# Performance work log

Measured on AMD Instinct MI355X. Metric: run time of the kernel, lower is better.

## Reference

```python
import jax, jax.numpy as jnp
import numpy as np

NUM_RELATIONS = 8
NUM_BASES = 4
IN_CH, HID, OUT_CH = 128, 64, 64
N_NODES, N_EDGES = 50000, 500000


def rgcn_conv(x, edge_src, edge_dst, edge_type, basis, comp, root, bias):
    """PyG RGCNConv with basis decomposition and per-relation mean aggregation.
    basis: [B, in, out], comp: [R, B], root: [in, out], bias: [out].
    W_r = sum_b comp[r, b] * basis[b]; msg_e = x[src_e] @ W_{type_e};
    aggregate mean over incoming edges per (node, relation), sum over relations,
    then add root transform and bias.
    """
    n = x.shape[0]
    out_dim = basis.shape[2]
    # Project once through all bases: [N, B, out]  (cheap: B=4)
    h = jnp.einsum('ni,bio->nbo', x, basis)
    # Per-edge message: contract gathered basis features with per-edge comp coeffs
    msg = jnp.einsum('eb,ebo->eo', comp[edge_type], h[edge_src])  # [E, out]
    # Mean aggregation per (dst, relation): segment id = dst*R + relation
    seg = edge_dst * NUM_RELATIONS + edge_type
    sums = jax.ops.segment_sum(msg, seg, num_segments=n * NUM_RELATIONS)
    cnt = jax.ops.segment_sum(jnp.ones((msg.shape[0], 1), msg.dtype), seg,
                              num_segments=n * NUM_RELATIONS)
    mean = sums / jnp.maximum(cnt, 1.0)
    agg = mean.reshape(n, NUM_RELATIONS, out_dim).sum(axis=1)
    return agg + x @ root + bias


def setup_inputs() -> dict:
    key = jax.random.key(0)
    ks = jax.random.split(key, 12)
    s1 = 1.0 / np.sqrt(IN_CH)
    s2 = 1.0 / np.sqrt(HID)
    return {
        'x': jax.random.normal(ks[0], (N_NODES, IN_CH), jnp.float32),
        'edge_index': jax.random.randint(ks[1], (2, N_EDGES), 0, N_NODES, jnp.int64),
        'edge_type': jax.random.randint(ks[2], (N_EDGES,), 0, NUM_RELATIONS, jnp.int64),
        'basis1': jax.random.normal(ks[3], (NUM_BASES, IN_CH, HID), jnp.float32) * s1,
        'comp1': jax.random.normal(ks[4], (NUM_RELATIONS, NUM_BASES), jnp.float32) * 0.5,
        'root1': jax.random.normal(ks[5], (IN_CH, HID), jnp.float32) * s1,
        'bias1': jnp.zeros((HID,), jnp.float32),
        'basis2': jax.random.normal(ks[6], (NUM_BASES, HID, OUT_CH), jnp.float32) * s2,
        'comp2': jax.random.normal(ks[7], (NUM_RELATIONS, NUM_BASES), jnp.float32) * 0.5,
        'root2': jax.random.normal(ks[8], (HID, OUT_CH), jnp.float32) * s2,
        'bias2': jnp.zeros((OUT_CH,), jnp.float32),
    }


def reference(x, edge_index, edge_type, basis1, comp1, root1, bias1,
              basis2, comp2, root2, bias2):
    src, dst = edge_index[0], edge_index[1]
    h = rgcn_conv(x, src, dst, edge_type, basis1, comp1, root1, bias1)
    h = jax.nn.relu(h)
    out = rgcn_conv(h, src, dst, edge_type, basis2, comp2, root2, bias2)
    return out
```

## Files before the change

kernel.cpp:

```cpp
#include <hip/hip_runtime.h>
#include <cstddef>

#define NREL 8
#define SCAN_TILE 4096

typedef __bf16 bf16x8 __attribute__((ext_vector_type(8)));
typedef float f32x4 __attribute__((ext_vector_type(4)));

__device__ __forceinline__ unsigned f2bf_u(float f) {
    unsigned u = __float_as_uint(f);
    u += 0x7FFFu + ((u >> 16) & 1u);
    return u >> 16;
}
__device__ __forceinline__ short f2bf(float f) { return (short)f2bf_u(f); }
__device__ __forceinline__ int pack2bf(float lo, float hi) {
    return (int)(f2bf_u(lo) | (f2bf_u(hi) << 16));
}
__device__ __forceinline__ float bfval(unsigned short g) {
    return __uint_as_float((unsigned)g << 16);
}

template<int K>
__device__ __forceinline__ void wfrag_body(const float* __restrict__ basis,
                                           const float* __restrict__ root,
                                           const float* __restrict__ comp,
                                           short* __restrict__ Wf, int tid)
{
    constexpr int NK = K / 32;
    int lane = tid & 63, slot = tid >> 6;
    int ks = slot % NK, t = slot / NK;
    int kg = lane >> 4, lr = lane & 15;
    int k0 = ks * 32 + kg * 8;
    union { short s[8]; int4 v; } u;
#pragma unroll
    for (int e = 0; e < 8; ++e) {
        int k = k0 + e;
        float v;
        if (t < 32) {
            int rr = t >> 2, ch = (t & 3) * 16 + lr;
            v = comp[rr * 4 + 0] * basis[((size_t)0 * K + k) * 64 + ch]
              + comp[rr * 4 + 1] * basis[((size_t)1 * K + k) * 64 + ch]
              + comp[rr * 4 + 2] * basis[((size_t)2 * K + k) * 64 + ch]
              + comp[rr * 4 + 3] * basis[((size_t)3 * K + k) * 64 + ch];
        } else {
            v = root[(size_t)k * 64 + (t - 32) * 16 + lr];
        }
        u.s[e] = f2bf(v);
    }
    *(int4*)(Wf + (size_t)tid * 8) = u.v;
}

__device__ __forceinline__ void afrag_body128(const float* __restrict__ x,
                                              short* __restrict__ xf, int N, int tid)
{
    int lane = tid & 63, slot = tid >> 6;
    int ks = slot & 3, rt = slot >> 2;
    int kg = lane >> 4, lr = lane & 15;
    int row = rt * 16 + lr, k = ks * 32 + kg * 8;
    union { short s[8]; int4 v; } u;
    if (row < N) {
        const float* xp = x + (size_t)row * 128 + k;
        float4 a = *(const float4*)xp;
        float4 b = *(const float4*)(xp + 4);
        u.s[0] = f2bf(a.x); u.s[1] = f2bf(a.y); u.s[2] = f2bf(a.z); u.s[3] = f2bf(a.w);
        u.s[4] = f2bf(b.x); u.s[5] = f2bf(b.y); u.s[6] = f2bf(b.z); u.s[7] = f2bf(b.w);
    } else {
        u.v = make_int4(0, 0, 0, 0);
    }
    *(int4*)(xf + (size_t)tid * 8) = u.v;
}

__global__ __launch_bounds__(256) void prep_kernel(
    const float* __restrict__ basis1, const float* __restrict__ root1,
    const float* __restrict__ comp1,  const float* __restrict__ basis2,
    const float* __restrict__ root2,  const float* __restrict__ comp2,
    const float* __restrict__ x,
    short* __restrict__ Wf1, short* __restrict__ Wf2, short* __restrict__ xf1,
    int4* __restrict__ zp, int zn16, int* __restrict__ offsN,
    int E, int N, int NT)
{
    int b = blockIdx.x;
    const int zb = (zn16 + 255) >> 8;
    if (b < zb) {
        int i = b * 256 + threadIdx.x;
        if (i < zn16) zp[i] = make_int4(0, 0, 0, 0);
        if (b == 0 && threadIdx.x == 0) *offsN = E;
        return;
    }
    b -= zb;
    if (b < 36) { wfrag_body<128>(basis1, root1, comp1, Wf1, b * 256 + threadIdx.x); return; }
    b -= 36;
    if (b < 18) { wfrag_body<64>(basis2, root2, comp2, Wf2, b * 256 + threadIdx.x); return; }
    b -= 18;
    int tid = b * 256 + threadIdx.x;
    if (tid < NT * 256) afrag_body128(x, xf1, N, tid);
}

__global__ __launch_bounds__(256) void hist_kernel(const int* __restrict__ dst,
                                                   const int* __restrict__ et,
                                                   int* __restrict__ cnt8, int E)
{
    int e = blockIdx.x * 256 + threadIdx.x;
    if (e < E) atomicAdd(&cnt8[dst[e] * NREL + et[e]], 1);
}

__global__ __launch_bounds__(256) void scan_part(const int* __restrict__ cnt8,
                                                 int* __restrict__ tsum, int n)
{
    int base = blockIdx.x * SCAN_TILE;
    int s = 0;
    for (int i = threadIdx.x; i < SCAN_TILE; i += 256) {
        int idx = base + i;
        if (idx < n) {
            int4 a = ((const int4*)cnt8)[idx * 2];
            int4 b = ((const int4*)cnt8)[idx * 2 + 1];
            s += a.x + a.y + a.z + a.w + b.x + b.y + b.z + b.w;
        }
    }
    for (int d = 1; d < 64; d <<= 1) s += __shfl_xor(s, d, 64);
    __shared__ int ws[4];
    if ((threadIdx.x & 63) == 0) ws[threadIdx.x >> 6] = s;
    __syncthreads();
    if (threadIdx.x == 0) tsum[blockIdx.x] = ws[0] + ws[1] + ws[2] + ws[3];
}

__global__ __launch_bounds__(256) void scan_final(const int* __restrict__ cnt8,
                                                  const int* __restrict__ tsum,
                                                  int* __restrict__ offs, int n)
{
    const int lane = threadIdx.x & 63, wid = threadIdx.x >> 6;
    int tbase = 0;
    for (int i = 0; i < blockIdx.x; ++i) tbase += tsum[i];
    int base = blockIdx.x * SCAN_TILE + threadIdx.x * 16;
    int v[16]; int s = 0;
#pragma unroll
    for (int j = 0; j < 16; ++j) {
        int idx = base + j;
        int dv = 0;
        if (idx < n) {
            int4 a = ((const int4*)cnt8)[idx * 2];
            int4 b = ((const int4*)cnt8)[idx * 2 + 1];
            dv = a.x + a.y + a.z + a.w + b.x + b.y + b.z + b.w;
        }
        v[j] = dv; s += dv;
    }
    int inc = s;
    for (int d = 1; d < 64; d <<= 1) {
        int t = __shfl_up(inc, d, 64);
        if (lane >= d) inc += t;
    }
    __shared__ int wsum[4];
    if (lane == 63) wsum[wid] = inc;
    __syncthreads();
    int run = tbase + (inc - s);
    for (int k = 0; k < wid; ++k) run += wsum[k];
#pragma unroll
    for (int j = 0; j < 16; ++j) {
        int idx = base + j;
        if (idx < n) offs[idx] = run;
        run += v[j];
    }
}

__global__ __launch_bounds__(256) void scatter_kernel(const int* __restrict__ src,
                                                      const int* __restrict__ dst,
                                                      const int* __restrict__ et,
                                                      const int* __restrict__ offs,
                                                      int* __restrict__ cursor,
                                                      const int* __restrict__ cnt8,
                                                      int2* __restrict__ edgeP, int E)
{
    int e = blockIdx.x * 256 + threadIdx.x;
    if (e >= E) return;
    int d = dst[e], r = et[e], s = src[e];
    int c = cnt8[d * NREL + r];
    float inv = 1.0f / (float)(c > 1 ? c : 1);
    int pos = offs[d] + atomicAdd(&cursor[d], 1);
    edgeP[pos] = make_int2(s * NREL + r, __float_as_int(inv));
}

template<int K>
__global__ __launch_bounds__(256) void gemm_mfma(const short* __restrict__ xf,
                                                 const short* __restrict__ Wf,
                                                 const float* __restrict__ bias,
                                                 short* __restrict__ hr,
                                                 float* __restrict__ yinit,
                                                 int N, int gblk)
{
    constexpr int NK = K / 32;
    __shared__ short lds[12 * NK * 512];

    const int w = threadIdx.x >> 6, lane = threadIdx.x & 63;
    const int kg = lane >> 4, lr = lane & 15;
    const int g0 = blockIdx.y * 3;

    {
        const int4* gsrc = (const int4*)(Wf + (size_t)g0 * 4 * NK * 512);
        int4* ldst = (int4*)lds;
        for (int i = threadIdx.x; i < 12 * NK * 64; i += 256)
            ldst[i] = gsrc[i];
    }

    float b0 = bias[lr], b1 = bias[16 + lr], b2 = bias[32 + lr], b3 = bias[48 + lr];

    __syncthreads();

    for (int bx = blockIdx.x; bx < gblk; bx += gridDim.x) {
        const int rt = bx * 4 + w;

        bf16x8 afrag[NK];
        const short* ap = xf + ((size_t)rt * NK * 64 + lane) * 8;
#pragma unroll
        for (int ks = 0; ks < NK; ++ks)
            afrag[ks] = *(const bf16x8*)(ap + ks * 512);

        f32x4 acc[12];
#pragma unroll
        for (int t = 0; t < 12; ++t) acc[t] = (f32x4){0.f, 0.f, 0.f, 0.f};

#pragma unroll
        for (int tt = 0; tt < 12; ++tt) {
#pragma unroll
            for (int ks = 0; ks < NK; ++ks) {
                bf16x8 bfrag = *(const bf16x8*)(lds + (tt * NK + ks) * 512 + lane * 8);
                acc[tt] = __builtin_amdgcn_mfma_f32_16x16x32_bf16(afrag[ks], bfrag,
                                                                  acc[tt], 0, 0, 0);
            }
        }

        const int drow0 = rt * 16 + kg * 4;
#pragma unroll
        for (int r = 0; r < 4; ++r) {
            int dr = drow0 + r;
            if (dr >= N) break;
#pragma unroll
            for (int gg = 0; gg < 3; ++gg) {
                int g = g0 + gg;
                if (g < 8) {
                    int u0 = pack2bf(acc[gg * 4 + 0][r], acc[gg * 4 + 1][r]);
                    int u1 = pack2bf(acc[gg * 4 + 2][r], acc[gg * 4 + 3][r]);
                    *(int2*)(hr + (size_t)dr * 512 + g * 64 + lr * 4) = make_int2(u0, u1);
                } else {
                    float4 o = make_float4(acc[gg * 4 + 0][r] + b0, acc[gg * 4 + 1][r] + b1,
                                           acc[gg * 4 + 2][r] + b2, acc[gg * 4 + 3][r] + b3);
                    *(float4*)(yinit + (size_t)dr * 64 + lr * 4) = o;
                }
            }
        }
    }
}

template<bool BF16OUT>
__global__ __launch_bounds__(256) void agg_kernel(const int* __restrict__ offs,
                                                  const int2* __restrict__ edgeP,
                                                  const short* __restrict__ hr,
                                                  const float* __restrict__ init,
                                                  float* __restrict__ outF,
                                                  short* __restrict__ outB, int N)
{
    const int dst = blockIdx.x * 4 + (threadIdx.x >> 6);
    const int l = threadIdx.x & 63;
    if (dst >= N) return;

    const unsigned short* hp = (const unsigned short*)hr;
    float acc = init[(size_t)dst * 64 + l];
    int e0 = offs[dst], e1 = offs[dst + 1];

    int e = e0;
    for (; e + 3 < e1; e += 4) {
        int2 p0 = edgeP[e],     p1 = edgeP[e + 1];
        int2 p2 = edgeP[e + 2], p3 = edgeP[e + 3];
        unsigned short g0 = hp[(size_t)p0.x * 64 + l];
        unsigned short g1 = hp[(size_t)p1.x * 64 + l];
        unsigned short g2 = hp[(size_t)p2.x * 64 + l];
        unsigned short g3 = hp[(size_t)p3.x * 64 + l];
        acc = fmaf(bfval(g0), __int_as_float(p0.y), acc);
        acc = fmaf(bfval(g1), __int_as_float(p1.y), acc);
        acc = fmaf(bfval(g2), __int_as_float(p2.y), acc);
        acc = fmaf(bfval(g3), __int_as_float(p3.y), acc);
    }
    for (; e < e1; ++e) {
        int2 p0 = edgeP[e];
        unsigned short g0 = hp[(size_t)p0.x * 64 + l];
        acc = fmaf(bfval(g0), __int_as_float(p0.y), acc);
    }

    int tc = (l & 3) * 16 + (l >> 2);
    if (BF16OUT) {
        int rt2 = dst >> 4, lr2 = dst & 15;
        int ks2 = tc >> 5, kg2 = (tc >> 3) & 3, e2 = tc & 7;
        outB[(((size_t)rt2 * 2 + ks2) * 64 + kg2 * 16 + lr2) * 8 + e2] =
            f2bf(fmaxf(acc, 0.f));
    } else {
        outF[(size_t)dst * 64 + tc] = acc;
    }
}

extern "C" void kernel_launch(void* const* d_in, const int* in_sizes, int n_in,
                              void* d_out, int out_size, void* d_ws, size_t ws_size,
                              hipStream_t stream)
{
    const float* x      = (const float*)d_in[0];
    const int*   ei     = (const int*)d_in[1];
    const int*   et     = (const int*)d_in[2];
    const float* basis1 = (const float*)d_in[3];
    const float* comp1  = (const float*)d_in[4];
    const float* root1  = (const float*)d_in[5];
    const float* bias1  = (const float*)d_in[6];
    const float* basis2 = (const float*)d_in[7];
    const float* comp2  = (const float*)d_in[8];
    const float* root2  = (const float*)d_in[9];
    const float* bias2  = (const float*)d_in[10];
    float* out = (float*)d_out;

    const int N = in_sizes[0] / 128;
    const int E = in_sizes[2];
    const int* src  = ei;
    const int* dstp = ei + E;

    const int gblk = (N + 63) / 64;
    const int NT   = gblk * 4;
    const int ablk = (N + 3) / 4;

    char* p = (char*)d_ws;
    auto carve = [&](size_t bytes) -> char* {
        char* q = p; p += (bytes + 255) & ~(size_t)255; return q;
    };
    int*   cursor  = (int*)carve((size_t)N * 4);
    int*   cnt8    = (int*)carve((size_t)N * NREL * 4);
    char*  zend    = p;
    int*   offs    = (int*)carve((size_t)(N + 1) * 4);
    int*   tsum    = (int*)carve(256 * 4);
    int2*  edgeP   = (int2*)carve((size_t)E * 8);
    short* Wf1     = (short*)carve((size_t)36 * 4 * 64 * 8 * 2);
    short* Wf2     = (short*)carve((size_t)36 * 2 * 64 * 8 * 2);
    float* yinit   = (float*)carve((size_t)N * 64 * 4);
    short* xf1     = (short*)carve((size_t)NT * 4 * 64 * 8 * 2);
    short* xf2     = (short*)carve((size_t)NT * 2 * 64 * 8 * 2);
    short* hr      = (short*)carve((size_t)N * 512 * 2);

    const int zn16 = (int)((zend - (char*)cursor) / 16);
    const int zb   = (zn16 + 255) / 256;
    const int ntiles = (N + SCAN_TILE - 1) / SCAN_TILE;

    prep_kernel<<<zb + 36 + 18 + NT, 256, 0, stream>>>(
        basis1, root1, comp1, basis2, root2, comp2, x,
        Wf1, Wf2, xf1, (int4*)cursor, zn16, offs + N, E, N, NT);

    hist_kernel<<<(E + 255) / 256, 256, 0, stream>>>(dstp, et, cnt8, E);
    scan_part<<<ntiles, 256, 0, stream>>>(cnt8, tsum, N);
    scan_final<<<ntiles, 256, 0, stream>>>(cnt8, tsum, offs, N);
    scatter_kernel<<<(E + 255) / 256, 256, 0, stream>>>(src, dstp, et, offs, cursor,
                                                        cnt8, edgeP, E);

    gemm_mfma<128><<<dim3(196, 3), 256, 0, stream>>>(xf1, Wf1, bias1, hr, yinit, N, gblk);
    agg_kernel<true><<<ablk, 256, 0, stream>>>(offs, edgeP, hr, yinit, nullptr, xf2, N);

    gemm_mfma<64><<<dim3(196, 3), 256, 0, stream>>>(xf2, Wf2, bias2, hr, yinit, N, gblk);
    agg_kernel<false><<<ablk, 256, 0, stream>>>(offs, edgeP, hr, yinit, out, nullptr, N);
}
```

Baseline: 189.8 us.

## Fuse histogram into prep, scatter with GEMM1, split edges across waves

Moves zeroing into its own kernel so the edge histogram can run inside the prep kernel. The edge scatter is fused with the first GEMM, which is made non-persistent and reads weight fragments straight from global memory instead of staging them in LDS. The root-plus-bias term is stored as bf16 instead of fp32, which cuts bandwidth at some precision cost. Aggregation now uses two waves per destination node that split the edge list and combine through LDS, aiming for more parallel gathers on nodes with many edges.

```diff
diff --git a/kernel.cpp b/kernel.cpp
--- a/kernel.cpp
+++ b/kernel.cpp
@@ -18,6 +18,14 @@
 }
 __device__ __forceinline__ float bfval(unsigned short g) {
     return __uint_as_float((unsigned)g << 16);
+}
+
+__global__ __launch_bounds__(256) void zero_kernel(int4* __restrict__ p, int n16,
+                                                   int* __restrict__ offsN, int E)
+{
+    int i = blockIdx.x * 256 + threadIdx.x;
+    if (i < n16) p[i] = make_int4(0, 0, 0, 0);
+    if (i == 0) *offsN = E;
 }
 
 template<int K>
@@ -70,38 +78,28 @@
     *(int4*)(xf + (size_t)tid * 8) = u.v;
 }
 
-__global__ __launch_bounds__(256) void prep_kernel(
+__global__ __launch_bounds__(256) void prep_hist_kernel(
+    const int* __restrict__ dstp, const int* __restrict__ et, int* __restrict__ cnt8,
     const float* __restrict__ basis1, const float* __restrict__ root1,
     const float* __restrict__ comp1,  const float* __restrict__ basis2,
     const float* __restrict__ root2,  const float* __restrict__ comp2,
     const float* __restrict__ x,
     short* __restrict__ Wf1, short* __restrict__ Wf2, short* __restrict__ xf1,
-    int4* __restrict__ zp, int zn16, int* __restrict__ offsN,
-    int E, int N, int NT)
+    int E, int N, int NT, int HB)
 {
     int b = blockIdx.x;
-    const int zb = (zn16 + 255) >> 8;
-    if (b < zb) {
-        int i = b * 256 + threadIdx.x;
-        if (i < zn16) zp[i] = make_int4(0, 0, 0, 0);
-        if (b == 0 && threadIdx.x == 0) *offsN = E;
+    if (b < HB) {
+        int e = b * 256 + threadIdx.x;
+        if (e < E) atomicAdd(&cnt8[dstp[e] * NREL + et[e]], 1);
         return;
     }
-    b -= zb;
+    b -= HB;
     if (b < 36) { wfrag_body<128>(basis1, root1, comp1, Wf1, b * 256 + threadIdx.x); return; }
     b -= 36;
     if (b < 18) { wfrag_body<64>(basis2, root2, comp2, Wf2, b * 256 + threadIdx.x); return; }
     b -= 18;
     int tid = b * 256 + threadIdx.x;
     if (tid < NT * 256) afrag_body128(x, xf1, N, tid);
-}
-
-__global__ __launch_bounds__(256) void hist_kernel(const int* __restrict__ dst,
-                                                   const int* __restrict__ et,
-                                                   int* __restrict__ cnt8, int E)
-{
-    int e = blockIdx.x * 256 + threadIdx.x;
-    if (e < E) atomicAdd(&cnt8[dst[e] * NREL + et[e]], 1);
 }
 
 __global__ __launch_bounds__(256) void scan_part(const int* __restrict__ cnt8,
@@ -162,128 +160,133 @@
     }
 }
 
-__global__ __launch_bounds__(256) void scatter_kernel(const int* __restrict__ src,
-                                                      const int* __restrict__ dst,
-                                                      const int* __restrict__ et,
-                                                      const int* __restrict__ offs,
-                                                      int* __restrict__ cursor,
-                                                      const int* __restrict__ cnt8,
-                                                      int2* __restrict__ edgeP, int E)
-{
-    int e = blockIdx.x * 256 + threadIdx.x;
-    if (e >= E) return;
-    int d = dst[e], r = et[e], s = src[e];
-    int c = cnt8[d * NREL + r];
-    float inv = 1.0f / (float)(c > 1 ? c : 1);
-    int pos = offs[d] + atomicAdd(&cursor[d], 1);
-    edgeP[pos] = make_int2(s * NREL + r, __float_as_int(inv));
-}
-
 template<int K>
-__global__ __launch_bounds__(256) void gemm_mfma(const short* __restrict__ xf,
-                                                 const short* __restrict__ Wf,
-                                                 const float* __restrict__ bias,
-                                                 short* __restrict__ hr,
-                                                 float* __restrict__ yinit,
-                                                 int N, int gblk)
+__device__ __forceinline__ void gemm_body(const short* __restrict__ xf,
+                                          const short* __restrict__ Wf,
+                                          const float* __restrict__ bias,
+                                          short* __restrict__ hr,
+                                          short* __restrict__ yb,
+                                          int N, int bx, int by)
 {
     constexpr int NK = K / 32;
-    __shared__ short lds[12 * NK * 512];
-
     const int w = threadIdx.x >> 6, lane = threadIdx.x & 63;
     const int kg = lane >> 4, lr = lane & 15;
-    const int g0 = blockIdx.y * 3;
-
-    {
-        const int4* gsrc = (const int4*)(Wf + (size_t)g0 * 4 * NK * 512);
-        int4* ldst = (int4*)lds;
-        for (int i = threadIdx.x; i < 12 * NK * 64; i += 256)
-            ldst[i] = gsrc[i];
+    const int rt = bx * 4 + w;
+    const int g0 = by * 3;
+
+    bf16x8 afrag[NK];
+    const short* ap = xf + ((size_t)rt * NK * 64 + lane) * 8;
+#pragma unroll
+    for (int ks = 0; ks < NK; ++ks)
+        afrag[ks] = *(const bf16x8*)(ap + ks * 512);
+
+    f32x4 acc[12];
+#pragma unroll
+    for (int t = 0; t < 12; ++t) acc[t] = (f32x4){0.f, 0.f, 0.f, 0.f};
+
+    const short* bp = Wf + ((size_t)g0 * 4 * NK * 64 + lane) * 8;
+#pragma unroll
+    for (int tt = 0; tt < 12; ++tt) {
+#pragma unroll
+        for (int ks = 0; ks < NK; ++ks) {
+            bf16x8 bfrag = *(const bf16x8*)(bp + (size_t)(tt * NK + ks) * 512);
+            acc[tt] = __builtin_amdgcn_mfma_f32_16x16x32_bf16(afrag[ks], bfrag,
+                                                              acc[tt], 0, 0, 0);
+        }
     }
 
     float b0 = bias[lr], b1 = bias[16 + lr], b2 = bias[32 + lr], b3 = bias[48 + lr];
 
-    __syncthreads();
-
-    for (int bx = blockIdx.x; bx < gblk; bx += gridDim.x) {
-        const int rt = bx * 4 + w;
-
-        bf16x8 afrag[NK];
-        const short* ap = xf + ((size_t)rt * NK * 64 + lane) * 8;
-#pragma unroll
-        for (int ks = 0; ks < NK; ++ks)
-            afrag[ks] = *(const bf16x8*)(ap + ks * 512);
-
-        f32x4 acc[12];
-#pragma unroll
-        for (int t = 0; t < 12; ++t) acc[t] = (f32x4){0.f, 0.f, 0.f, 0.f};
-
-#pragma unroll
-        for (int tt = 0; tt < 12; ++tt) {
-#pragma unroll
-            for (int ks = 0; ks < NK; ++ks) {
-                bf16x8 bfrag = *(const bf16x8*)(lds + (tt * NK + ks) * 512 + lane * 8);
-                acc[tt] = __builtin_amdgcn_mfma_f32_16x16x32_bf16(afrag[ks], bfrag,
-                                                                  acc[tt], 0, 0, 0);
+    const int drow0 = rt * 16 + kg * 4;
+#pragma unroll
+    for (int r = 0; r < 4; ++r) {
+        int dr = drow0 + r;
+        if (dr >= N) break;
+#pragma unroll
+        for (int gg = 0; gg < 3; ++gg) {
+            int g = g0 + gg;
+            if (g < 8) {
+                int u0 = pack2bf(acc[gg * 4 + 0][r], acc[gg * 4 + 1][r]);
+                int u1 = pack2bf(acc[gg * 4 + 2][r], acc[gg * 4 + 3][r]);
+                *(int2*)(hr + (size_t)dr * 512 + g * 64 + lr * 4) = make_int2(u0, u1);
+            } else {
+                int u0 = pack2bf(acc[gg * 4 + 0][r] + b0, acc[gg * 4 + 1][r] + b1);
+                int u1 = pack2bf(acc[gg * 4 + 2][r] + b2, acc[gg * 4 + 3][r] + b3);
+                *(int2*)(yb + (size_t)dr * 64 + lr * 4) = make_int2(u0, u1);
             }
         }
-
-        const int drow0 = rt * 16 + kg * 4;
-#pragma unroll
-        for (int r = 0; r < 4; ++r) {
-            int dr = drow0 + r;
-            if (dr >= N) break;
-#pragma unroll
-            for (int gg = 0; gg < 3; ++gg) {
-                int g = g0 + gg;
-                if (g < 8) {
-                    int u0 = pack2bf(acc[gg * 4 + 0][r], acc[gg * 4 + 1][r]);
-                    int u1 = pack2bf(acc[gg * 4 + 2][r], acc[gg * 4 + 3][r]);
-                    *(int2*)(hr + (size_t)dr * 512 + g * 64 + lr * 4) = make_int2(u0, u1);
-                } else {
-                    float4 o = make_float4(acc[gg * 4 + 0][r] + b0, acc[gg * 4 + 1][r] + b1,
-                                           acc[gg * 4 + 2][r] + b2, acc[gg * 4 + 3][r] + b3);
-                    *(float4*)(yinit + (size_t)dr * 64 + lr * 4) = o;
-                }
-            }
-        }
-    }
+    }
+}
+
+__global__ __launch_bounds__(256) void scatter_gemm1_kernel(
+    const int* __restrict__ src, const int* __restrict__ dstp,
+    const int* __restrict__ et,  const int* __restrict__ offs,
+    int* __restrict__ cursor,    const int* __restrict__ cnt8,
+    int2* __restrict__ edgeP,    int E, int SB,
+    const short* __restrict__ xf1, const short* __restrict__ Wf1,
+    const float* __restrict__ bias1, short* __restrict__ hr,
+    short* __restrict__ yb, int N, int gblk)
+{
+    if (blockIdx.x < SB) {
+        int e = blockIdx.x * 256 + threadIdx.x;
+        if (e >= E) return;
+        int d = dstp[e], r = et[e], s = src[e];
+        int c = cnt8[d * NREL + r];
+        float inv = 1.0f / (float)(c > 1 ? c : 1);
+        int pos = offs[d] + atomicAdd(&cursor[d], 1);
+        edgeP[pos] = make_int2(s * NREL + r, __float_as_int(inv));
+        return;
+    }
+    int b = blockIdx.x - SB;
+    gemm_body<128>(xf1, Wf1, bias1, hr, yb, N, b % gblk, b / gblk);
+}
+
+__global__ __launch_bounds__(256) void gemm2_kernel(const short* __restrict__ xf,
+                                                    const short* __restrict__ Wf,
+                                                    const float* __restrict__ bias,
+                                                    short* __restrict__ hr,
+                                                    short* __restrict__ yb, int N)
+{
+    gemm_body<64>(xf, Wf, bias, hr, yb, N, blockIdx.x, blockIdx.y);
 }
 
 template<bool BF16OUT>
 __global__ __launch_bounds__(256) void agg_kernel(const int* __restrict__ offs,
                                                   const int2* __restrict__ edgeP,
                                                   const short* __restrict__ hr,
-                                                  const float* __restrict__ init,
+                                                  const short* __restrict__ yb,
                                                   float* __restrict__ outF,
                                                   short* __restrict__ outB, int N)
 {
-    const int dst = blockIdx.x * 4 + (threadIdx.x >> 6);
-    const int l = threadIdx.x & 63;
-    if (dst >= N) return;
+    __shared__ float red[2][64];
+    const int w = threadIdx.x >> 6, l = threadIdx.x & 63;
+    const int ds = w >> 1, sub = w & 1;
+    const int dst = blockIdx.x * 2 + ds;
 
     const unsigned short* hp = (const unsigned short*)hr;
-    float acc = init[(size_t)dst * 64 + l];
-    int e0 = offs[dst], e1 = offs[dst + 1];
-
-    int e = e0;
-    for (; e + 3 < e1; e += 4) {
-        int2 p0 = edgeP[e],     p1 = edgeP[e + 1];
-        int2 p2 = edgeP[e + 2], p3 = edgeP[e + 3];
-        unsigned short g0 = hp[(size_t)p0.x * 64 + l];
-        unsigned short g1 = hp[(size_t)p1.x * 64 + l];
-        unsigned short g2 = hp[(size_t)p2.x * 64 + l];
-        unsigned short g3 = hp[(size_t)p3.x * 64 + l];
-        acc = fmaf(bfval(g0), __int_as_float(p0.y), acc);
-        acc = fmaf(bfval(g1), __int_as_float(p1.y), acc);
-        acc = fmaf(bfval(g2), __int_as_float(p2.y), acc);
-        acc = fmaf(bfval(g3), __int_as_float(p3.y), acc);
-    }
-    for (; e < e1; ++e) {
-        int2 p0 = edgeP[e];
-        unsigned short g0 = hp[(size_t)p0.x * 64 + l];
-        acc = fmaf(bfval(g0), __int_as_float(p0.y), acc);
-    }
+    float acc = 0.f;
+    if (dst < N) {
+        int e0 = offs[dst], e1 = offs[dst + 1];
+        int e = e0 + sub;
+        for (; e + 2 < e1; e += 4) {
+            int2 p0 = edgeP[e], p1 = edgeP[e + 2];
+            unsigned short g0 = hp[(size_t)p0.x * 64 + l];
+            unsigned short g1 = hp[(size_t)p1.x * 64 + l];
+            acc = fmaf(bfval(g0), __int_as_float(p0.y), acc);
+            acc = fmaf(bfval(g1), __int_as_float(p1.y), acc);
+        }
+        if (e < e1) {
+            int2 p0 = edgeP[e];
+            unsigned short g0 = hp[(size_t)p0.x * 64 + l];
+            acc = fmaf(bfval(g0), __int_as_float(p0.y), acc);
+        }
+    }
+    if (sub == 1) red[ds][l] = acc;
+    __syncthreads();
+    if (sub == 1 || dst >= N) return;
+
+    acc += red[ds][l];
+    acc += bfval(((const unsigned short*)yb)[(size_t)dst * 64 + l]);
 
     int tc = (l & 3) * 16 + (l >> 2);
     if (BF16OUT) {
@@ -320,7 +323,7 @@
 
     const int gblk = (N + 63) / 64;
     const int NT   = gblk * 4;
-    const int ablk = (N + 3) / 4;
+    const int HB   = (E + 255) / 256;
 
     char* p = (char*)d_ws;
     auto carve = [&](size_t bytes) -> char* {
@@ -334,28 +337,32 @@
     int2*  edgeP   = (int2*)carve((size_t)E * 8);
     short* Wf1     = (short*)carve((size_t)36 * 4 * 64 * 8 * 2);
     short* Wf2     = (short*)carve((size_t)36 * 2 * 64 * 8 * 2);
-    float* yinit   = (float*)carve((size_t)N * 64 * 4);
+    short* yb      = (short*)carve((size_t)N * 64 * 2);
     short* xf1     = (short*)carve((size_t)NT * 4 * 64 * 8 * 2);
     short* xf2     = (short*)carve((size_t)NT * 2 * 64 * 8 * 2);
     short* hr      = (short*)carve((size_t)N * 512 * 2);
 
     const int zn16 = (int)((zend - (char*)cursor) / 16);
-    const int zb   = (zn16 + 255) / 256;
     const int ntiles = (N + SCAN_TILE - 1) / SCAN_TILE;
 
-    prep_kernel<<<zb + 36 + 18 + NT, 256, 0, stream>>>(
-        basis1, root1, comp1, basis2, root2, comp2, x,
-        Wf1, Wf2, xf1, (int4*)cursor, zn16, offs + N, E, N, NT);
-
-    hist_kernel<<<(E + 255) / 256, 256, 0, stream>>>(dstp, et, cnt8, E);
+    zero_kernel<<<(zn16 + 255) / 256, 256, 0, stream>>>((int4*)cursor, zn16, offs + N, E);
+
+    prep_hist_kernel<<<HB + 36 + 18 + NT, 256, 0, stream>>>(
+        dstp, et, cnt8, basis1, root1, comp1, basis2, root2, comp2, x,
+        Wf1, Wf2, xf1, E, N, NT, HB);
+
     scan_part<<<ntiles, 256, 0, stream>>>(cnt8, tsum, N);
     scan_final<<<ntiles, 256, 0, stream>>>(cnt8, tsum, offs, N);
-    scatter_kernel<<<(E + 255) / 256, 256, 0, stream>>>(src, dstp, et, offs, cursor,
-                                                        cnt8, edgeP, E);
-
-    gemm_mfma<128><<<dim3(196, 3), 256, 0, stream>>>(xf1, Wf1, bias1, hr, yinit, N, gblk);
-    agg_kernel<true><<<ablk, 256, 0, stream>>>(offs, edgeP, hr, yinit, nullptr, xf2, N);
-
-    gemm_mfma<64><<<dim3(196, 3), 256, 0, stream>>>(xf2, Wf2, bias2, hr, yinit, N, gblk);
-    agg_kernel<false><<<ablk, 256, 0, stream>>>(offs, edgeP, hr, yinit, out, nullptr, N);
-}
+
+    scatter_gemm1_kernel<<<HB + gblk * 3, 256, 0, stream>>>(
+        src, dstp, et, offs, cursor, cnt8, edgeP, E, HB,
+        xf1, Wf1, bias1, hr, yb, N, gblk);
+
+    agg_kernel<true><<<(N + 1) / 2, 256, 0, stream>>>(offs, edgeP, hr, yb,
+                                                      nullptr, xf2, N);
+
+    gemm2_kernel<<<dim3(gblk, 3), 256, 0, stream>>>(xf2, Wf2, bias2, hr, yb, N);
+
+    agg_kernel<false><<<(N + 1) / 2, 256, 0, stream>>>(offs, edgeP, hr, yb,
+                                                       out, nullptr, N);
+}
```

After: 206.6 us. 8.8% more time.
